# Kernel optimization log

Hardware: AMD Instinct MI355X
Metric: run time of the kernel (lower is better)

Reference implementation:

```python
import jax, jax.numpy as jnp
import numpy as np

EPS = 1e-06
ITERS = 10


def _dilate(x):
    # 3x3 max-pool, stride 1, same padding; torch pads max_pool with -inf
    return jax.lax.reduce_window(x, -jnp.inf, jax.lax.max,
                                 (1, 1, 3, 3), (1, 1, 1, 1), 'SAME')


def _erode(x):
    return -_dilate(-x)


def _soft_skeletonize(img, iters=ITERS):
    skel = jnp.zeros_like(img)
    for _ in range(iters):
        opened = _dilate(_erode(img))
        delta = jax.nn.relu(img - opened)
        skel = skel + jax.nn.relu(delta - skel)
        img = _erode(img)
    return skel


def setup_inputs() -> dict:
    key = jax.random.key(0)
    k1, k2 = jax.random.split(key)
    pred_prob = jax.random.normal(k1, (32, 1, 1024, 1024), dtype=jnp.float32)
    gt_onehot = jax.random.uniform(k2, (32, 1, 1024, 1024), dtype=jnp.float32)
    return {"pred_prob": pred_prob, "gt_onehot": gt_onehot}


def reference(pred_prob, gt_onehot):
    # binary branch: C == 1, logits -> sigmoid
    p = jax.nn.sigmoid(pred_prob)
    skel_pred = _soft_skeletonize(p, ITERS)
    skel_gt = _soft_skeletonize(gt_onehot, ITERS)
    tprec = jnp.sum(skel_pred * gt_onehot, axis=(2, 3)) / (jnp.sum(skel_pred, axis=(2, 3)) + EPS)
    tsens = jnp.sum(skel_gt * p, axis=(2, 3)) / (jnp.sum(skel_gt, axis=(2, 3)) + EPS)
    cldice = 2 * tprec * tsens / (tprec + tsens + EPS)
    return 1.0 - jnp.mean(cldice)
```

## Files before the change

kernel.cpp:

```cpp
#include <hip/hip_runtime.h>
#include <math.h>


typedef unsigned int u32;
typedef _Float16 h2 __attribute__((ext_vector_type(2)));

#define STRD 52
#define BB   0x7BFF7BFFu
#define NB   0xFBFFFBFFu

__device__ __forceinline__ u32 ab(u32 hi, u32 lo) {
  return __builtin_amdgcn_alignbit(hi, lo, 16);
}
__device__ __forceinline__ u32 bcu(h2 x) { return __builtin_bit_cast(u32, x); }
__device__ __forceinline__ h2  bch(u32 x) { return __builtin_bit_cast(h2, x); }
__device__ __forceinline__ u32 pmin(u32 a, u32 b) {
  return bcu(__builtin_elementwise_min(bch(a), bch(b)));
}
__device__ __forceinline__ u32 pmax(u32 a, u32 b) {
  return bcu(__builtin_elementwise_max(bch(a), bch(b)));
}
__device__ __forceinline__ u32 pmin3(u32 a, u32 b, u32 c) { return pmin(pmin(a, b), c); }
__device__ __forceinline__ u32 pmax3(u32 a, u32 b, u32 c) { return pmax(pmax(a, b), c); }
__device__ __forceinline__ u32 skup(u32 sk, u32 im, u32 op) {
  h2 d = bch(im) - bch(op);
  return bcu(__builtin_elementwise_max(bch(sk), d));
}
__device__ __forceinline__ float sigmoidf_(float x) {
  return 1.0f / (1.0f + __expf(-x));
}

__device__ __forceinline__ void load12(const u32* __restrict__ p,
                                       u32* __restrict__ r) {
  uint4 a = *(const uint4*)p;
  uint4 b = *(const uint4*)(p + 4);
  uint4 c = *(const uint4*)(p + 8);
  r[0]=a.x; r[1]=a.y; r[2]=a.z; r[3]=a.w;
  r[4]=b.x; r[5]=b.y; r[6]=b.z; r[7]=b.w;
  r[8]=c.x; r[9]=c.y; r[10]=c.z; r[11]=c.w;
}

__device__ __forceinline__ void store12(u32* __restrict__ q,
                                        const u32* __restrict__ r) {
  *(uint4*)(q)     = make_uint4(r[0], r[1], r[2],  r[3]);
  *(uint4*)(q + 4) = make_uint4(r[4], r[5], r[6],  r[7]);
  *(uint4*)(q + 8) = make_uint4(r[8], r[9], r[10], r[11]);
}

__device__ __forceinline__ void hrow12(const u32* __restrict__ v,
                                       u32 hl, u32 hr,
                                       u32* __restrict__ o) {
  u32 m0 = ab(v[0], hl);
  #pragma unroll
  for (int i = 0; i < 12; ++i) {
    u32 m1 = (i < 11) ? ab(v[i + 1], v[i]) : ab(hr, v[11]);
    o[i] = pmin3(m0, v[i], m1);
    m0 = m1;
  }
}

template <bool FIRST>
__device__ __forceinline__ void erode_phase(
    const u32* __restrict__ P, u32* __restrict__ Q,
    int as3, int eoff, int pu, int pd, bool c0, bool c3, int ph,
    u32* __restrict__ e0, u32* __restrict__ e1, u32* __restrict__ e2)
{
  if (as3 + 2 < 6 + ph || as3 > 89 - ph) return;
  const u32* pr = P + (as3 - 1) * STRD + eoff;
  u32 rT[12], rB[12];
  load12(pr, rT);
  if (FIRST) {
    load12(pr + STRD,     e0);
    load12(pr + 2 * STRD, e1);
    load12(pr + 3 * STRD, e2);
  }
  load12(pr + 4 * STRD, rB);
  u32 t[12], v0[12], v1[12], v2[12];
  #pragma unroll
  for (int i = 0; i < 12; ++i) t[i]  = pmin(e0[i], e1[i]);
  #pragma unroll
  for (int i = 0; i < 12; ++i) v0[i] = pmin(rT[i], t[i]);
  #pragma unroll
  for (int i = 0; i < 12; ++i) v1[i] = pmin(t[i], e2[i]);
  #pragma unroll
  for (int i = 0; i < 12; ++i) v2[i] = pmin(e1[i], pmin(e2[i], rB[i]));
  u32 hl0 = (u32)__builtin_amdgcn_ds_bpermute(pu, (int)v0[11]);
  u32 hr0 = (u32)__builtin_amdgcn_ds_bpermute(pd, (int)v0[0]);
  u32 hl1 = (u32)__builtin_amdgcn_ds_bpermute(pu, (int)v1[11]);
  u32 hr1 = (u32)__builtin_amdgcn_ds_bpermute(pd, (int)v1[0]);
  u32 hl2 = (u32)__builtin_amdgcn_ds_bpermute(pu, (int)v2[11]);
  u32 hr2 = (u32)__builtin_amdgcn_ds_bpermute(pd, (int)v2[0]);
  hl0 = c0 ? BB : hl0;  hr0 = c3 ? BB : hr0;
  hl1 = c0 ? BB : hl1;  hr1 = c3 ? BB : hr1;
  hl2 = c0 ? BB : hl2;  hr2 = c3 ? BB : hr2;
  u32* qw = Q + as3 * STRD + eoff;
  hrow12(v0, hl0, hr0, e0);  store12(qw,            e0);
  hrow12(v1, hl1, hr1, e1);  store12(qw + STRD,     e1);
  hrow12(v2, hl2, hr2, e2);  store12(qw + 2 * STRD, e2);
}

__device__ __forceinline__ void dilate_phase(
    const u32* __restrict__ P, const u32* __restrict__ NBR,
    int dr, int db, bool bu, bool bd, bool lfix, bool rfix,
    const u32* __restrict__ img, u32* __restrict__ imgn,
    u32* __restrict__ sk)
{
  const u32* pm = bu ? (P + (dr - 1) * STRD + db) : (NBR + db);
  const u32* pc = P + dr * STRD + db;
  const u32* pp = bd ? (P + (dr + 1) * STRD + db) : (NBR + db);
  u32 vm[21];
  #pragma unroll
  for (int j = 0; j < 6; ++j) {
    uint4 x = *(const uint4*)(pm + 4 * j);
    uint4 y = *(const uint4*)(pc + 4 * j);
    uint4 z = *(const uint4*)(pp + 4 * j);
    u32 xs[4] = {x.x, x.y, x.z, x.w};
    u32 ys[4] = {y.x, y.y, y.z, y.w};
    u32 zs[4] = {z.x, z.y, z.z, z.w};
    #pragma unroll
    for (int k = 0; k < 4; ++k) {
      int i = 4 * j + k;
      if (i >= 4 && i <= 19) imgn[i - 4] = ys[k];
      if (i >= 3 && i <= 20) vm[i] = pmax3(xs[k], ys[k], zs[k]);
    }
  }
  if (lfix) vm[3]  = (vm[3]  & 0x0000FFFFu) | 0xFBFF0000u;
  if (rfix) vm[20] = (vm[20] & 0xFFFF0000u) | 0x0000FBFFu;
  u32 m0 = ab(vm[4], vm[3]);
  #pragma unroll
  for (int i = 0; i < 16; ++i) {
    u32 m1 = ab(vm[i + 5], vm[i + 4]);
    u32 op = pmax3(m0, vm[i + 4], m1);
    m0 = m1;
    sk[i] = skup(sk[i], img[i], op);
  }
}

__global__ __launch_bounds__(256, 4) void skel_tile_kernel(
    const float* __restrict__ pred, const float* __restrict__ gt,
    float* __restrict__ sums)
{
  __shared__ __align__(16) u32 L[STRD * 196];
  u32* const Ad = L + STRD;
  u32* const Bd = L + STRD * 98;
  const u32* const NBR = L + STRD * 195;

  const int tile = blockIdx.x;
  const int b    = blockIdx.y;
  const int s    = blockIdx.z;
  const int txI = tile & 15, tyI = tile >> 4;
  const int x0 = txI * 64 - 16, y0 = tyI * 64 - 16;
  const int t  = threadIdx.x;
  const size_t base = (size_t)b << 20;
  const float* __restrict__ src  = s ? gt   : pred;
  const float* __restrict__ osrc = s ? pred : gt;

  for (int i = t; i < STRD; i += 256) L[STRD * 195 + i] = NB;

  for (int i = t; i < 86 * 12; i += 256) {
    int ci = i % 12, row = i / 12 + 5;
    int gy = y0 + row, gx0 = x0 + ci * 8;
    uint4 hv;
    if ((unsigned)gy < 1024u && gx0 >= 0 && gx0 + 8 <= 1024) {
      const size_t g = base + (size_t)gy * 1024 + gx0;
      const float4 f0 = *(const float4*)&src[g];
      const float4 f1 = *(const float4*)&src[g + 4];
      float ff[8] = {f0.x, f0.y, f0.z, f0.w, f1.x, f1.y, f1.z, f1.w};
      u32 d[4];
      #pragma unroll
      for (int e = 0; e < 4; ++e) {
        float a = ff[2 * e], bb2 = ff[2 * e + 1];
        if (s == 0) { a = sigmoidf_(a); bb2 = sigmoidf_(bb2); }
        h2 p; p[0] = (_Float16)a; p[1] = (_Float16)bb2;
        d[e] = bcu(p);
      }
      hv = make_uint4(d[0], d[1], d[2], d[3]);
    } else {
      u32 d[4];
      #pragma unroll
      for (int e = 0; e < 4; ++e) {
        float va = 65504.0f, vb = 65504.0f;
        int gxa = gx0 + 2 * e, gxb = gxa + 1;
        if ((unsigned)gy < 1024u && (unsigned)gxa < 1024u) {
          va = src[base + (size_t)gy * 1024 + gxa];
          if (s == 0) va = sigmoidf_(va);
        }
        if ((unsigned)gy < 1024u && (unsigned)gxb < 1024u) {
          vb = src[base + (size_t)gy * 1024 + gxb];
          if (s == 0) vb = sigmoidf_(vb);
        }
        h2 p; p[0] = (_Float16)va; p[1] = (_Float16)vb;
        d[e] = bcu(p);
      }
      hv = make_uint4(d[0], d[1], d[2], d[3]);
    }
    *(uint4*)&Ad[row * STRD + ci * 4] = hv;
  }
  __syncthreads();

  const int lane = t & 63, wid = t >> 6;

  const int seg = t >> 2, ec = t & 3;
  const int as3 = 3 * seg;
  const bool c0 = (ec == 0), c3 = (ec == 3);
  const int pu = ((lane - 1) & 63) * 4;
  const int pd = ((lane + 1) & 63) * 4;
  const int eoff = 12 * ec;

  const int q  = wid - 2;
  const int dr = 16 + lane;
  const int db = 4 + 16 * q;
  const int gyD = y0 + dr;
  const bool bu = (gyD >= 1), bd = (gyD <= 1022);
  const bool lfix = (q == 0) && (txI == 0);
  const bool rfix = (q == 1) && (txI == 15);

  u32 st[48];
  u32* const e0 = st;
  u32* const e1 = st + 12;
  u32* const e2 = st + 24;
  u32* const iA = st;
  u32* const iB = st + 16;
  u32* const sk = st + 32;
  #pragma unroll
  for (int i = 0; i < 16; ++i) sk[i] = 0;

  if (wid < 2) {
    erode_phase<true>(Ad, Bd, as3, eoff, pu, pd, c0, c3, 0, e0, e1, e2);
  } else {
    const u32* p = Ad + dr * STRD + db;
    #pragma unroll
    for (int i = 0; i < 4; ++i) {
      uint4 v = *(const uint4*)(p + 4 + 4 * i);
      iA[4*i] = v.x; iA[4*i+1] = v.y; iA[4*i+2] = v.z; iA[4*i+3] = v.w;
    }
  }
  __syncthreads();

  #pragma unroll 1
  for (int it = 1; it <= 9; it += 2) {
    if (wid < 2) {
      erode_phase<false>(Bd, Ad, as3, eoff, pu, pd, c0, c3, it, e0, e1, e2);
    } else {
      dilate_phase(Bd, NBR, dr, db, bu, bd, lfix, rfix, iA, iB, sk);
    }
    __syncthreads();
    if (wid < 2) {
      if (it < 9)
        erode_phase<false>(Ad, Bd, as3, eoff, pu, pd, c0, c3, it + 1,
                           e0, e1, e2);
    } else {
      dilate_phase(Ad, NBR, dr, db, bu, bd, lfix, rfix, iB, iA, sk);
    }
    __syncthreads();
  }

  float s0 = 0.f, s1 = 0.f;
  if (wid >= 2) {
    const int gxb = x0 + 2 * db + 8;
    const size_t g = base + (size_t)gyD * 1024 + gxb;
    #pragma unroll
    for (int v4i = 0; v4i < 8; ++v4i) {
      const float4 f = *(const float4*)&osrc[g + 4 * v4i];
      float o0 = f.x, o1 = f.y, o2 = f.z, o3 = f.w;
      if (s == 1) {
        o0 = sigmoidf_(o0); o1 = sigmoidf_(o1);
        o2 = sigmoidf_(o2); o3 = sigmoidf_(o3);
      }
      h2 qa = bch(sk[2 * v4i]);
      h2 qb = bch(sk[2 * v4i + 1]);
      float a0 = (float)qa[0], a1 = (float)qa[1];
      float a2 = (float)qb[0], a3 = (float)qb[1];
      s0 += a0 * o0 + a1 * o1 + a2 * o2 + a3 * o3;
      s1 += a0 + a1 + a2 + a3;
    }
  }
  for (int off = 32; off >= 1; off >>= 1) {
    s0 += __shfl_down(s0, off, 64);
    s1 += __shfl_down(s1, off, 64);
  }
  float* red = (float*)L;
  if (lane == 0) { red[wid * 2] = s0; red[wid * 2 + 1] = s1; }
  __syncthreads();
  if (t == 0) {
    atomicAdd(&sums[(s * 32 + b) * 2 + 0], red[4] + red[6]);
    atomicAdd(&sums[(s * 32 + b) * 2 + 1], red[5] + red[7]);
  }
}

__global__ void finalize_kernel(const float* __restrict__ sums,
                                float* __restrict__ out)
{
  const int t = threadIdx.x;
  float cl = 0.f;
  if (t < 32) {
    float pn = sums[t * 2 + 0],        pd = sums[t * 2 + 1];
    float sn = sums[(32 + t) * 2 + 0], sd = sums[(32 + t) * 2 + 1];
    float tprec = pn / (pd + 1e-6f);
    float tsens = sn / (sd + 1e-6f);
    cl = 2.f * tprec * tsens / (tprec + tsens + 1e-6f);
  }
  for (int off = 32; off >= 1; off >>= 1) cl += __shfl_down(cl, off, 64);
  if (t == 0) out[0] = 1.f - cl / 32.f;
}

extern "C" void kernel_launch(void* const* d_in, const int* in_sizes, int n_in,
                              void* d_out, int out_size, void* d_ws, size_t ws_size,
                              hipStream_t stream) {
  const float* pred = (const float*)d_in[0];
  const float* gt   = (const float*)d_in[1];
  float* sums = (float*)d_ws;
  hipMemsetAsync(sums, 0, 128 * sizeof(float), stream);
  dim3 grid(256, 32, 2);
  skel_tile_kernel<<<grid, dim3(256), 0, stream>>>(pred, gt, sums);
  finalize_kernel<<<1, 64, 0, stream>>>(sums, (float*)d_out);
}
```

Measured before the change: 652.2 us.

## Use single in-place LDS buffer for erosion to raise occupancy

Replaces the ping-pong double LDS buffers with one in-place buffer. Erosion results are computed into registers, followed by a barrier, then stored back, which roughly halves shared memory per block. Launch bounds go from 4 to 8 blocks per CU. This roughly doubles the number of __syncthreads per iteration and puts the stores on the critical path. It also raises register pressure, since the 256x8 launch bound caps VGPRs while the kernel holds 48+ u32 state per thread.

```diff
diff --git a/kernel.cpp b/kernel.cpp
--- a/kernel.cpp
+++ b/kernel.cpp
@@ -60,13 +60,12 @@
 }
 
 template <bool FIRST>
-__device__ __forceinline__ void erode_phase(
-    const u32* __restrict__ P, u32* __restrict__ Q,
-    int as3, int eoff, int pu, int pd, bool c0, bool c3, int ph,
+__device__ __forceinline__ void erode_compute(
+    const u32* __restrict__ E,
+    int as3, int eoff, int pu, int pd, bool c0, bool c3,
     u32* __restrict__ e0, u32* __restrict__ e1, u32* __restrict__ e2)
 {
-  if (as3 + 2 < 6 + ph || as3 > 89 - ph) return;
-  const u32* pr = P + (as3 - 1) * STRD + eoff;
+  const u32* pr = E + (as3 - 1) * STRD + eoff;
   u32 rT[12], rB[12];
   load12(pr, rT);
   if (FIRST) {
@@ -93,21 +92,31 @@
   hl0 = c0 ? BB : hl0;  hr0 = c3 ? BB : hr0;
   hl1 = c0 ? BB : hl1;  hr1 = c3 ? BB : hr1;
   hl2 = c0 ? BB : hl2;  hr2 = c3 ? BB : hr2;
-  u32* qw = Q + as3 * STRD + eoff;
-  hrow12(v0, hl0, hr0, e0);  store12(qw,            e0);
-  hrow12(v1, hl1, hr1, e1);  store12(qw + STRD,     e1);
-  hrow12(v2, hl2, hr2, e2);  store12(qw + 2 * STRD, e2);
+  hrow12(v0, hl0, hr0, e0);
+  hrow12(v1, hl1, hr1, e1);
+  hrow12(v2, hl2, hr2, e2);
+}
+
+__device__ __forceinline__ void erode_store(
+    u32* __restrict__ E, int as3, int eoff,
+    const u32* __restrict__ e0, const u32* __restrict__ e1,
+    const u32* __restrict__ e2)
+{
+  u32* qw = E + as3 * STRD + eoff;
+  store12(qw,            e0);
+  store12(qw + STRD,     e1);
+  store12(qw + 2 * STRD, e2);
 }
 
 __device__ __forceinline__ void dilate_phase(
-    const u32* __restrict__ P, const u32* __restrict__ NBR,
+    const u32* __restrict__ E, const u32* __restrict__ NBR,
     int dr, int db, bool bu, bool bd, bool lfix, bool rfix,
     const u32* __restrict__ img, u32* __restrict__ imgn,
     u32* __restrict__ sk)
 {
-  const u32* pm = bu ? (P + (dr - 1) * STRD + db) : (NBR + db);
-  const u32* pc = P + dr * STRD + db;
-  const u32* pp = bd ? (P + (dr + 1) * STRD + db) : (NBR + db);
+  const u32* pm = bu ? (E + (dr - 1) * STRD + db) : (NBR + db);
+  const u32* pc = E + dr * STRD + db;
+  const u32* pp = bd ? (E + (dr + 1) * STRD + db) : (NBR + db);
   u32 vm[21];
   #pragma unroll
   for (int j = 0; j < 6; ++j) {
@@ -136,14 +145,13 @@
   }
 }
 
-__global__ __launch_bounds__(256, 4) void skel_tile_kernel(
+__global__ __launch_bounds__(256, 8) void skel_tile_kernel(
     const float* __restrict__ pred, const float* __restrict__ gt,
     float* __restrict__ sums)
 {
-  __shared__ __align__(16) u32 L[STRD * 196];
-  u32* const Ad = L + STRD;
-  u32* const Bd = L + STRD * 98;
-  const u32* const NBR = L + STRD * 195;
+  __shared__ __align__(16) u32 L[STRD * 97];
+  u32* const E = L;
+  const u32* const NBR = L + STRD * 96;
 
   const int tile = blockIdx.x;
   const int b    = blockIdx.y;
@@ -155,7 +163,7 @@
   const float* __restrict__ src  = s ? gt   : pred;
   const float* __restrict__ osrc = s ? pred : gt;
 
-  for (int i = t; i < STRD; i += 256) L[STRD * 195 + i] = NB;
+  for (int i = t; i < STRD; i += 256) L[STRD * 96 + i] = NB;
 
   for (int i = t; i < 86 * 12; i += 256) {
     int ci = i % 12, row = i / 12 + 5;
@@ -194,7 +202,7 @@
       }
       hv = make_uint4(d[0], d[1], d[2], d[3]);
     }
-    *(uint4*)&Ad[row * STRD + ci * 4] = hv;
+    *(uint4*)&E[row * STRD + ci * 4] = hv;
   }
   __syncthreads();
 
@@ -225,10 +233,11 @@
   #pragma unroll
   for (int i = 0; i < 16; ++i) sk[i] = 0;
 
+  const bool a0 = !(as3 + 2 < 6 || as3 > 89);
   if (wid < 2) {
-    erode_phase<true>(Ad, Bd, as3, eoff, pu, pd, c0, c3, 0, e0, e1, e2);
+    if (a0) erode_compute<true>(E, as3, eoff, pu, pd, c0, c3, e0, e1, e2);
   } else {
-    const u32* p = Ad + dr * STRD + db;
+    const u32* p = E + dr * STRD + db;
     #pragma unroll
     for (int i = 0; i < 4; ++i) {
       uint4 v = *(const uint4*)(p + 4 + 4 * i);
@@ -236,22 +245,29 @@
     }
   }
   __syncthreads();
+  if (wid < 2 && a0) erode_store(E, as3, eoff, e0, e1, e2);
+  __syncthreads();
 
   #pragma unroll 1
   for (int it = 1; it <= 9; it += 2) {
+    const bool a1 = !(as3 + 2 < 6 + it || as3 > 89 - it);
+    const bool a2 = !(as3 + 2 < 7 + it || as3 > 88 - it);
     if (wid < 2) {
-      erode_phase<false>(Bd, Ad, as3, eoff, pu, pd, c0, c3, it, e0, e1, e2);
+      if (a1) erode_compute<false>(E, as3, eoff, pu, pd, c0, c3, e0, e1, e2);
     } else {
-      dilate_phase(Bd, NBR, dr, db, bu, bd, lfix, rfix, iA, iB, sk);
-    }
+      dilate_phase(E, NBR, dr, db, bu, bd, lfix, rfix, iA, iB, sk);
+    }
+    __syncthreads();
+    if (wid < 2 && a1) erode_store(E, as3, eoff, e0, e1, e2);
     __syncthreads();
     if (wid < 2) {
-      if (it < 9)
-        erode_phase<false>(Ad, Bd, as3, eoff, pu, pd, c0, c3, it + 1,
-                           e0, e1, e2);
+      if (it < 9 && a2)
+        erode_compute<false>(E, as3, eoff, pu, pd, c0, c3, e0, e1, e2);
     } else {
-      dilate_phase(Ad, NBR, dr, db, bu, bd, lfix, rfix, iB, iA, sk);
-    }
+      dilate_phase(E, NBR, dr, db, bu, bd, lfix, rfix, iB, iA, sk);
+    }
+    __syncthreads();
+    if (wid < 2 && it < 9 && a2) erode_store(E, as3, eoff, e0, e1, e2);
     __syncthreads();
   }
 
```

After: 953.3 us. +46.2%, slower.
